# Performance work log

Hardware: AMD Instinct MI355X
Metric: run time of the kernel (lower is better)

Reference implementation:

```python
import jax, jax.numpy as jnp
import numpy as np

N = 50000      # nodes
E = 800000     # edges
F_IN = 128     # input node features
HID = 96       # hidden_channels (heads=1 -> in_dim=HID)
L = 4          # num_layers
OUT = 1
EPS_SM = 1e-16 # PyG softmax eps


def layer_norm(x, g, b):
    mu = jnp.mean(x, axis=-1, keepdims=True)
    var = jnp.var(x, axis=-1, keepdims=True)
    return (x - mu) * jax.lax.rsqrt(var + 1e-5) * g + b


def gatv2_layer(h, src, dst, ea, Wl, bl, Wr, br, We, att, bias):
    # GATv2Conv, heads=1, concat=True, add_self_loops=False, edge_dim=1
    xl = h @ Wl + bl                      # [N, C] source transform (x_j)
    xr = h @ Wr + br                      # [N, C] target transform (x_i)
    e = xl[src] + xr[dst] + ea @ We       # [E, C]
    e = jax.nn.leaky_relu(e, 0.2)
    alpha = e @ att                       # [E]
    # softmax over incoming edges of each destination node
    m = jax.ops.segment_max(alpha, dst, num_segments=N)
    a = jnp.exp(alpha - m[dst])
    s = jax.ops.segment_sum(a, dst, num_segments=N)
    a = a / (s[dst] + EPS_SM)
    out = jax.ops.segment_sum(xl[src] * a[:, None], dst, num_segments=N)
    return out + bias


def setup_inputs() -> dict:
    key = jax.random.key(0)
    ks = jax.random.split(key, 24)
    sc_in = 1.0 / np.sqrt(F_IN)
    sc_h = 1.0 / np.sqrt(HID)
    inp = {
        "x": jax.random.normal(ks[0], (N, F_IN), jnp.float32),
        "edge_index": jax.random.randint(ks[1], (2, E), 0, N, jnp.int64),
        "edge_weight": jax.random.uniform(ks[2], (E,), jnp.float32),
        "enc_W": jax.random.normal(ks[3], (F_IN, HID), jnp.float32) * sc_in,
        "enc_b": jnp.zeros((HID,), jnp.float32),
        "Wl": jax.random.normal(ks[4], (L, HID, HID), jnp.float32) * sc_h,
        "bl": jnp.zeros((L, HID), jnp.float32),
        "Wr": jax.random.normal(ks[5], (L, HID, HID), jnp.float32) * sc_h,
        "br": jnp.zeros((L, HID), jnp.float32),
        "We": jax.random.normal(ks[6], (L, 1, HID), jnp.float32),
        "att": jax.random.normal(ks[7], (L, HID), jnp.float32) * sc_h,
        "bias": jnp.zeros((L, HID), jnp.float32),
        "ln_g": jnp.ones((L, HID), jnp.float32),
        "ln_b": jnp.zeros((L, HID), jnp.float32),
        "lnf_g": jnp.ones((HID,), jnp.float32),
        "lnf_b": jnp.zeros((HID,), jnp.float32),
        "fc_W": jax.random.normal(ks[8], (HID, OUT), jnp.float32) * sc_h,
        "fc_b": jnp.zeros((OUT,), jnp.float32),
    }
    return inp


def reference(x, edge_index, edge_weight, enc_W, enc_b, Wl, bl, Wr, br, We, att,
              bias, ln_g, ln_b, lnf_g, lnf_b, fc_W, fc_b):
    src, dst = edge_index[0], edge_index[1]
    ea = edge_weight[:, None]             # [E, 1] edge_attr
    h = x @ enc_W + enc_b                 # node encoder
    for i in range(L):                    # DeepGCNLayer block='res+'
        hn = jax.nn.relu(layer_norm(h, ln_g[i], ln_b[i]))
        h = h + gatv2_layer(hn, src, dst, ea, Wl[i], bl[i], Wr[i], br[i],
                            We[i], att[i], bias[i])
    h = jax.nn.relu(layer_norm(h, lnf_g, lnf_b))
    return h @ fc_W + fc_b
```

## Files before the change

kernel.cpp:

```cpp
#include <hip/hip_runtime.h>
#include <math.h>

#define NN 50000
#define EE 800000
#define FIN 128
#define HID 96
#define NL 4
#define CHUNK 1024

typedef __attribute__((ext_vector_type(8))) short short8;
typedef __attribute__((ext_vector_type(4))) float floatx4;
typedef __attribute__((ext_vector_type(2))) _Float16 half2v;

#define WPREP_L (NL * 2 * 9216)
#define WPREP_TOT (WPREP_L + 12288)

__device__ __forceinline__ unsigned short f32_to_bf16_rne(float x) {
    unsigned u = __float_as_uint(x);
    unsigned r = (u + 0x7FFFu + ((u >> 16) & 1u)) >> 16;
    return (unsigned short)r;
}
__device__ __forceinline__ float bf16_to_f32(unsigned short h) {
    return __uint_as_float(((unsigned)h) << 16);
}

__global__ void k_hist(const int* __restrict__ dst, int* __restrict__ deg, int E) {
    int e = blockIdx.x * blockDim.x + threadIdx.x;
    if (e < E) atomicAdd(&deg[dst[e]], 1);
}

__global__ void k_scan1(const int* __restrict__ deg, int* __restrict__ partials, int n) {
    __shared__ int lds[256];
    int t = threadIdx.x;
    int base = blockIdx.x * CHUNK + t * 4;
    int s = 0;
    #pragma unroll
    for (int q = 0; q < 4; q++) { int idx = base + q; if (idx < n) s += deg[idx]; }
    lds[t] = s; __syncthreads();
    for (int o = 128; o > 0; o >>= 1) { if (t < o) lds[t] += lds[t + o]; __syncthreads(); }
    if (t == 0) partials[blockIdx.x] = lds[0];
}

__global__ void k_scan_mid(int* partials, int nb, int* rowptr, int n) {
    int lane = threadIdx.x;
    int orig = (lane < nb) ? partials[lane] : 0;
    int v = orig;
    #pragma unroll
    for (int off = 1; off < 64; off <<= 1) {
        int u = __shfl_up(v, off);
        if (lane >= off) v += u;
    }
    if (lane < nb) partials[lane] = v - orig;
    if (lane == 63) rowptr[n] = v;
}

__global__ void k_scan3(const int* __restrict__ deg, const int* __restrict__ partials,
                        int* __restrict__ rowptr, int* __restrict__ cursor, int n) {
    __shared__ int lds[256];
    int t = threadIdx.x;
    int base = blockIdx.x * CHUNK + t * 4;
    int v[4];
    #pragma unroll
    for (int q = 0; q < 4; q++) { int idx = base + q; v[q] = (idx < n) ? deg[idx] : 0; }
    int tsum = v[0] + v[1] + v[2] + v[3];
    lds[t] = tsum; __syncthreads();
    for (int o = 1; o < 256; o <<= 1) {
        int add = (t >= o) ? lds[t - o] : 0;
        __syncthreads();
        lds[t] += add;
        __syncthreads();
    }
    int excl = lds[t] - tsum;
    int run = partials[blockIdx.x] + excl;
    #pragma unroll
    for (int q = 0; q < 4; q++) {
        int idx = base + q;
        if (idx < n) { rowptr[idx] = run; cursor[idx] = run; run += v[q]; }
    }
}

__global__ void k_scatter(const int* __restrict__ src, const int* __restrict__ dst,
                          const float* __restrict__ ew, int* __restrict__ cursor,
                          uint2* __restrict__ epack, int E) {
    int e = blockIdx.x * blockDim.x + threadIdx.x;
    if (e < E) {
        int p = atomicAdd(&cursor[dst[e]], 1);
        epack[p] = make_uint2((unsigned)src[e], __float_as_uint(ew[e]));
    }
}

__global__ void k_wprep_all(const float* __restrict__ Wl, const float* __restrict__ Wr,
                            const float* __restrict__ encW,
                            unsigned short* __restrict__ wf_hi, unsigned short* __restrict__ wf_lo,
                            unsigned short* __restrict__ we_hi, unsigned short* __restrict__ we_lo) {
    int t = blockIdx.x * blockDim.x + threadIdx.x;
    if (t < WPREP_L) {
        int within = t % 9216, pair = t / 9216;
        int lr = pair & 1, layer = pair >> 1;
        int j = within & 7;
        int lane = (within >> 3) & 63;
        int cs = within >> 9;
        int s = cs % 3, ct = cs / 3;
        int col = ct * 16 + (lane & 15);
        int k = s * 32 + (lane >> 4) * 8 + j;
        const float* W = (lr ? Wr : Wl) + (size_t)layer * HID * HID;
        float v = W[k * HID + col];
        unsigned short hi = f32_to_bf16_rne(v);
        wf_hi[t] = hi;
        wf_lo[t] = f32_to_bf16_rne(v - bf16_to_f32(hi));
    } else if (t < WPREP_TOT) {
        int u = t - WPREP_L;
        int j = u & 7;
        int lane = (u >> 3) & 63;
        int cs = u >> 9;
        int s = cs & 3, ct = cs >> 2;
        int col = ct * 16 + (lane & 15);
        int k = s * 32 + (lane >> 4) * 8 + j;
        float v = encW[k * HID + col];
        unsigned short hi = f32_to_bf16_rne(v);
        we_hi[u] = hi;
        we_lo[u] = f32_to_bf16_rne(v - bf16_to_f32(hi));
    }
}

__global__ __launch_bounds__(256) void k_enc_mfma(const float* __restrict__ x,
        const unsigned short* __restrict__ we_hi, const unsigned short* __restrict__ we_lo,
        const float* __restrict__ b,
        const float* __restrict__ lng, const float* __restrict__ lnb,
        float* __restrict__ h,
        unsigned short* __restrict__ hn_hi, unsigned short* __restrict__ hn_lo, int n) {
    int t = threadIdx.x;
    int wave = t >> 6, lane = t & 63;
    int quad = lane >> 4, lid = lane & 15;
    int r0 = blockIdx.x * 64 + wave * 16;
    int arow = r0 + lid; if (arow >= n) arow = n - 1;
    short8 aH[4], aL[4];
    #pragma unroll
    for (int s = 0; s < 4; s++) {
        float4 p0 = *(const float4*)(x + (size_t)arow * FIN + s * 32 + quad * 8);
        float4 p1 = *(const float4*)(x + (size_t)arow * FIN + s * 32 + quad * 8 + 4);
        float f[8] = {p0.x, p0.y, p0.z, p0.w, p1.x, p1.y, p1.z, p1.w};
        #pragma unroll
        for (int j = 0; j < 8; j++) {
            unsigned short hi = f32_to_bf16_rne(f[j]);
            aH[s][j] = (short)hi;
            aL[s][j] = (short)f32_to_bf16_rne(f[j] - bf16_to_f32(hi));
        }
    }
    floatx4 o[6];
    #pragma unroll
    for (int ct = 0; ct < 6; ct++) {
        floatx4 acc = {0.f, 0.f, 0.f, 0.f};
        #pragma unroll
        for (int s = 0; s < 4; s++) {
            short8 bH = *(const short8*)(we_hi + ((ct * 4 + s) * 64 + lane) * 8);
            short8 bL = *(const short8*)(we_lo + ((ct * 4 + s) * 64 + lane) * 8);
            acc = __builtin_amdgcn_mfma_f32_16x16x32_bf16(aH[s], bH, acc, 0, 0, 0);
            acc = __builtin_amdgcn_mfma_f32_16x16x32_bf16(aH[s], bL, acc, 0, 0, 0);
            acc = __builtin_amdgcn_mfma_f32_16x16x32_bf16(aL[s], bH, acc, 0, 0, 0);
        }
        float bv = b[ct * 16 + lid];
        #pragma unroll
        for (int rg = 0; rg < 4; rg++) o[ct][rg] = acc[rg] + bv;
    }
    #pragma unroll
    for (int rg = 0; rg < 4; rg++) {
        float s1 = 0.f, s2 = 0.f;
        #pragma unroll
        for (int ct = 0; ct < 6; ct++) { s1 += o[ct][rg]; s2 += o[ct][rg] * o[ct][rg]; }
        #pragma unroll
        for (int off = 1; off < 16; off <<= 1) {
            s1 += __shfl_xor(s1, off);
            s2 += __shfl_xor(s2, off);
        }
        float mu = s1 * (1.f / 96.f);
        float var = s2 * (1.f / 96.f) - mu * mu;
        float rs = rsqrtf(var + 1e-5f);
        int orow = r0 + quad * 4 + rg;
        if (orow < n) {
            #pragma unroll
            for (int ct = 0; ct < 6; ct++) {
                int col = ct * 16 + lid;
                float v = o[ct][rg];
                h[(size_t)orow * HID + col] = v;
                float y = fmaxf((v - mu) * rs * lng[col] + lnb[col], 0.f);
                unsigned short hi = f32_to_bf16_rne(y);
                hn_hi[(size_t)orow * HID + col] = hi;
                hn_lo[(size_t)orow * HID + col] = f32_to_bf16_rne(y - bf16_to_f32(hi));
            }
        }
    }
}

__global__ __launch_bounds__(256) void k_gemm2_mfma(
        const unsigned short* __restrict__ hn_hi, const unsigned short* __restrict__ hn_lo,
        const unsigned short* __restrict__ wf_hi, const unsigned short* __restrict__ wf_lo,
        const float* __restrict__ bl, const float* __restrict__ br,
        unsigned short* __restrict__ xl_h, unsigned short* __restrict__ xr_h, int n) {
    int t = threadIdx.x;
    int wave = t >> 6, lane = t & 63;
    int quad = lane >> 4, lid = lane & 15;
    int r0 = blockIdx.x * 64 + wave * 16;
    int arow = r0 + lid; if (arow >= n) arow = n - 1;
    short8 aH[3], aL[3];
    #pragma unroll
    for (int s = 0; s < 3; s++) {
        aH[s] = *(const short8*)(hn_hi + (size_t)arow * HID + s * 32 + quad * 8);
        aL[s] = *(const short8*)(hn_lo + (size_t)arow * HID + s * 32 + quad * 8);
    }
    #pragma unroll
    for (int lr = 0; lr < 2; lr++) {
        const unsigned short* sh = wf_hi + lr * 9216;
        const unsigned short* sl = wf_lo + lr * 9216;
        const float* bias = lr ? br : bl;
        unsigned short* out = lr ? xr_h : xl_h;
        #pragma unroll
        for (int ct = 0; ct < 6; ct++) {
            floatx4 acc = {0.f, 0.f, 0.f, 0.f};
            #pragma unroll
            for (int s = 0; s < 3; s++) {
                short8 bH = *(const short8*)(sh + ((ct * 3 + s) * 64 + lane) * 8);
                short8 bL = *(const short8*)(sl + ((ct * 3 + s) * 64 + lane) * 8);
                acc = __builtin_amdgcn_mfma_f32_16x16x32_bf16(aH[s], bH, acc, 0, 0, 0);
                acc = __builtin_amdgcn_mfma_f32_16x16x32_bf16(aH[s], bL, acc, 0, 0, 0);
                acc = __builtin_amdgcn_mfma_f32_16x16x32_bf16(aL[s], bH, acc, 0, 0, 0);
            }
            int col = ct * 16 + lid;
            float bv = bias[col];
            #pragma unroll
            for (int rg = 0; rg < 4; rg++) {
                int orow = r0 + quad * 4 + rg;
                if (orow < n) {
                    _Float16 hv = (_Float16)(acc[rg] + bv);
                    out[(size_t)orow * HID + col] = *(unsigned short*)&hv;
                }
            }
        }
    }
}

__global__ __launch_bounds__(256) void k_gat_fused(
        const unsigned short* __restrict__ xl_h, const unsigned short* __restrict__ xr_h,
        const uint2* __restrict__ ep, const int* __restrict__ rowptr,
        const float* __restrict__ We, const float* __restrict__ att, const float* __restrict__ bias,
        float* __restrict__ h,
        unsigned short* __restrict__ hn_hi, unsigned short* __restrict__ hn_lo,
        float* __restrict__ out_final,
        const float* __restrict__ g, const float* __restrict__ bt,
        const float* __restrict__ fcW, const float* __restrict__ fcb,
        int mode, int n) {
    int lane = threadIdx.x & 63;
    int node = blockIdx.x * 4 + (threadIdx.x >> 6);
    if (node >= n) return;
    int grp = lane >> 4, sub = lane & 15;
    bool act = sub < 12;
    int d0 = sub * 8;
    unsigned gOffB = (unsigned)((act ? sub : 11) * 16);

    const float LOG2E = 1.4426950408889634f;
    half2v we_h[4], at_h[4], xr_hv[4];
    {
        union U8i { uint4 u; half2v h2[4]; };
        U8i xrw;
        xrw.u = *(const uint4*)((const char*)xr_h + ((unsigned)node * 192u + gOffB));
        if (act) {
            float4 a0 = *(const float4*)(We + d0),  a1 = *(const float4*)(We + d0 + 4);
            float4 c0 = *(const float4*)(att + d0), c1 = *(const float4*)(att + d0 + 4);
            we_h[0] = half2v{(_Float16)a0.x, (_Float16)a0.y}; we_h[1] = half2v{(_Float16)a0.z, (_Float16)a0.w};
            we_h[2] = half2v{(_Float16)a1.x, (_Float16)a1.y}; we_h[3] = half2v{(_Float16)a1.z, (_Float16)a1.w};
            at_h[0] = half2v{(_Float16)(c0.x*LOG2E), (_Float16)(c0.y*LOG2E)};
            at_h[1] = half2v{(_Float16)(c0.z*LOG2E), (_Float16)(c0.w*LOG2E)};
            at_h[2] = half2v{(_Float16)(c1.x*LOG2E), (_Float16)(c1.y*LOG2E)};
            at_h[3] = half2v{(_Float16)(c1.z*LOG2E), (_Float16)(c1.w*LOG2E)};
            #pragma unroll
            for (int j = 0; j < 4; j++) xr_hv[j] = xrw.h2[j];
        } else {
            #pragma unroll
            for (int j = 0; j < 4; j++) {
                we_h[j] = half2v{(_Float16)0.f, (_Float16)0.f};
                at_h[j] = we_h[j]; xr_hv[j] = we_h[j];
            }
        }
    }
    const half2v c02 = half2v{(_Float16)0.2f, (_Float16)0.2f};

    int beg = rowptr[node], end = rowptr[node + 1];
    float ssum = 0.f;
    float acc[8];
    #pragma unroll
    for (int j = 0; j < 8; j++) acc[j] = 0.f;

    union U8 { uint4 u; half2v h2[4]; _Float16 hf[8]; };

    auto lq = [&](int p, uint4& vraw, float& w, bool& val) {
        int pe = p + grp;
        val = pe < end;
        int pc = val ? pe : end - 1;
        uint2 e = ep[pc];
        w = __uint_as_float(e.y);
        vraw = *(const uint4*)((const char*)xl_h + (e.x * 192u + gOffB));
    };
    auto proc = [&](const uint4& vraw, float w, bool val) {
        U8 cv; cv.u = vraw;
        _Float16 wh = (_Float16)w;
        half2v w2 = half2v{wh, wh};
        float q = 0.f;
        #pragma unroll
        for (int j = 0; j < 4; j++) {
            half2v t = cv.h2[j] + xr_hv[j];
            t = w2 * we_h[j] + t;
            half2v t2 = t * c02;
            t = __builtin_elementwise_max(t, t2);
#if __has_builtin(__builtin_amdgcn_fdot2)
            q = __builtin_amdgcn_fdot2(t, at_h[j], q, false);
#else
            q = fmaf((float)t[0], (float)at_h[j][0], q);
            q = fmaf((float)t[1], (float)at_h[j][1], q);
#endif
        }
        q += __shfl_xor(q, 1); q += __shfl_xor(q, 2);
        q += __shfl_xor(q, 4); q += __shfl_xor(q, 8);
        float e = val ? exp2f(q) : 0.f;
        ssum += e;
        #pragma unroll
        for (int j = 0; j < 8; j++) acc[j] = fmaf((float)cv.hf[j], e, acc[j]);
    };

    if (beg < end) {
        uint4 vA, vB; float wA, wB; bool okA, okB;
        lq(beg,     vA, wA, okA);
        lq(beg + 4, vB, wB, okB);
        for (int p = beg; p < end; p += 8) {
            proc(vA, wA, okA);
            lq(p + 8, vA, wA, okA);
            proc(vB, wB, okB);
            lq(p + 12, vB, wB, okB);
        }
    }

    ssum += __shfl_xor(ssum, 16); ssum += __shfl_xor(ssum, 32);
    #pragma unroll
    for (int j = 0; j < 8; j++) {
        acc[j] += __shfl_xor(acc[j], 16);
        acc[j] += __shfl_xor(acc[j], 32);
    }
    float inv = 1.f / (ssum + 1e-16f);

    float nh[8];
    float s1 = 0.f, s2 = 0.f;
    if (act) {
        float4 h0 = *(const float4*)(h + (size_t)node * HID + d0);
        float4 h1 = *(const float4*)(h + (size_t)node * HID + d0 + 4);
        float4 b0 = *(const float4*)(bias + d0);
        float4 b1 = *(const float4*)(bias + d0 + 4);
        float hv[8] = {h0.x,h0.y,h0.z,h0.w,h1.x,h1.y,h1.z,h1.w};
        float bv[8] = {b0.x,b0.y,b0.z,b0.w,b1.x,b1.y,b1.z,b1.w};
        #pragma unroll
        for (int j = 0; j < 8; j++) {
            nh[j] = hv[j] + acc[j] * inv + bv[j];
            s1 += nh[j];
            s2 += nh[j] * nh[j];
        }
    } else {
        #pragma unroll
        for (int j = 0; j < 8; j++) nh[j] = 0.f;
    }
    #pragma unroll
    for (int off = 1; off < 16; off <<= 1) {
        s1 += __shfl_xor(s1, off);
        s2 += __shfl_xor(s2, off);
    }
    float mu = s1 * (1.f / 96.f);
    float var = s2 * (1.f / 96.f) - mu * mu;
    float rs = rsqrtf(var + 1e-5f);

    if (mode == 0) {
        if (grp == 0 && act) {
            float4 g0 = *(const float4*)(g + d0),  g1 = *(const float4*)(g + d0 + 4);
            float4 t0 = *(const float4*)(bt + d0), t1 = *(const float4*)(bt + d0 + 4);
            float gv[8] = {g0.x,g0.y,g0.z,g0.w,g1.x,g1.y,g1.z,g1.w};
            float tv[8] = {t0.x,t0.y,t0.z,t0.w,t1.x,t1.y,t1.z,t1.w};
            *(float4*)(h + (size_t)node * HID + d0)     = make_float4(nh[0], nh[1], nh[2], nh[3]);
            *(float4*)(h + (size_t)node * HID + d0 + 4) = make_float4(nh[4], nh[5], nh[6], nh[7]);
            unsigned hi[4], lo[4];
            #pragma unroll
            for (int j = 0; j < 4; j++) {
                float ox = fmaxf((nh[2*j]   - mu) * rs * gv[2*j]   + tv[2*j],   0.f);
                float oy = fmaxf((nh[2*j+1] - mu) * rs * gv[2*j+1] + tv[2*j+1], 0.f);
                unsigned short hx = f32_to_bf16_rne(ox), hy = f32_to_bf16_rne(oy);
                unsigned short lx = f32_to_bf16_rne(ox - bf16_to_f32(hx));
                unsigned short ly = f32_to_bf16_rne(oy - bf16_to_f32(hy));
                hi[j] = (unsigned)hx | ((unsigned)hy << 16);
                lo[j] = (unsigned)lx | ((unsigned)ly << 16);
            }
            *(uint4*)(hn_hi + (size_t)node * HID + d0) = make_uint4(hi[0], hi[1], hi[2], hi[3]);
            *(uint4*)(hn_lo + (size_t)node * HID + d0) = make_uint4(lo[0], lo[1], lo[2], lo[3]);
        }
    } else {
        float pacc = 0.f;
        if (act) {
            float4 g0 = *(const float4*)(g + d0),  g1 = *(const float4*)(g + d0 + 4);
            float4 t0 = *(const float4*)(bt + d0), t1 = *(const float4*)(bt + d0 + 4);
            float4 w0 = *(const float4*)(fcW + d0), w1 = *(const float4*)(fcW + d0 + 4);
            float gv[8] = {g0.x,g0.y,g0.z,g0.w,g1.x,g1.y,g1.z,g1.w};
            float tv[8] = {t0.x,t0.y,t0.z,t0.w,t1.x,t1.y,t1.z,t1.w};
            float wv[8] = {w0.x,w0.y,w0.z,w0.w,w1.x,w1.y,w1.z,w1.w};
            #pragma unroll
            for (int j = 0; j < 8; j++) {
                float y = fmaxf((nh[j] - mu) * rs * gv[j] + tv[j], 0.f);
                pacc = fmaf(y, wv[j], pacc);
            }
        }
        #pragma unroll
        for (int off = 1; off < 16; off <<= 1) pacc += __shfl_xor(pacc, off);
        if (lane == 0) out_final[node] = pacc + fcb[0];
    }
}

extern "C" void kernel_launch(void* const* d_in, const int* in_sizes, int n_in,
                              void* d_out, int out_size, void* d_ws, size_t ws_size,
                              hipStream_t stream) {
    const float* x    = (const float*)d_in[0];
    const int*   ei   = (const int*)  d_in[1];
    const float* ew   = (const float*)d_in[2];
    const float* encW = (const float*)d_in[3];
    const float* encB = (const float*)d_in[4];
    const float* Wl   = (const float*)d_in[5];
    const float* bl   = (const float*)d_in[6];
    const float* Wr   = (const float*)d_in[7];
    const float* br   = (const float*)d_in[8];
    const float* We   = (const float*)d_in[9];
    const float* att  = (const float*)d_in[10];
    const float* bias = (const float*)d_in[11];
    const float* lng  = (const float*)d_in[12];
    const float* lnb  = (const float*)d_in[13];
    const float* lnfg = (const float*)d_in[14];
    const float* lnfb = (const float*)d_in[15];
    const float* fcW  = (const float*)d_in[16];
    const float* fcb  = (const float*)d_in[17];
    float* out = (float*)d_out;

    const int* src = ei;
    const int* dst = ei + EE;

    char* ws = (char*)d_ws;
    size_t off = 0;
    auto alloc = [&](size_t bytes) -> void* {
        void* p = ws + off;
        off += (bytes + 255) & ~(size_t)255;
        return p;
    };
    float* h      = (float*)alloc((size_t)NN * HID * 4);
    unsigned short* xl_h  = (unsigned short*)alloc((size_t)NN * HID * 2 + 256);
    unsigned short* xr_h  = (unsigned short*)alloc((size_t)NN * HID * 2 + 256);
    unsigned short* hn_hi = (unsigned short*)alloc((size_t)NN * HID * 2);
    unsigned short* hn_lo = (unsigned short*)alloc((size_t)NN * HID * 2);
    unsigned short* wf_hi = (unsigned short*)alloc((size_t)WPREP_L * 2);
    unsigned short* wf_lo = (unsigned short*)alloc((size_t)WPREP_L * 2);
    unsigned short* we_hi = (unsigned short*)alloc(12288 * 2);
    unsigned short* we_lo = (unsigned short*)alloc(12288 * 2);
    int*   deg    = (int*)  alloc((size_t)NN * 4);
    int*   rowptr = (int*)  alloc((size_t)(NN + 1) * 4);
    int*   cursor = (int*)  alloc((size_t)NN * 4);
    uint2* epack  = (uint2*)alloc((size_t)EE * 8);
    int*   parts  = (int*)  alloc(256 * 4);

    const int NB = (NN + CHUNK - 1) / CHUNK;
    const int EB = (EE + 255) / 256;
    const int MB = (NN + 63) / 64;
    const int WB = (NN + 3) / 4;

    hipMemsetAsync(deg, 0, (size_t)NN * 4, stream);
    k_hist<<<EB, 256, 0, stream>>>(dst, deg, EE);
    k_scan1<<<NB, 256, 0, stream>>>(deg, parts, NN);
    k_scan_mid<<<1, 64, 0, stream>>>(parts, NB, rowptr, NN);
    k_scan3<<<NB, 256, 0, stream>>>(deg, parts, rowptr, cursor, NN);
    k_scatter<<<EB, 256, 0, stream>>>(src, dst, ew, cursor, epack, EE);

    k_wprep_all<<<(WPREP_TOT + 255) / 256, 256, 0, stream>>>(Wl, Wr, encW, wf_hi, wf_lo, we_hi, we_lo);

    k_enc_mfma<<<MB, 256, 0, stream>>>(x, we_hi, we_lo, encB, lng, lnb, h, hn_hi, hn_lo, NN);

    for (int l = 0; l < NL; l++) {
        k_gemm2_mfma<<<MB, 256, 0, stream>>>(hn_hi, hn_lo,
            wf_hi + (size_t)l * 2 * 9216, wf_lo + (size_t)l * 2 * 9216,
            bl + l * HID, br + l * HID, xl_h, xr_h, NN);
        if (l < NL - 1) {
            k_gat_fused<<<WB, 256, 0, stream>>>(xl_h, xr_h, epack, rowptr,
                We + l * HID, att + l * HID, bias + l * HID,
                h, hn_hi, hn_lo, (float*)nullptr,
                lng + (l + 1) * HID, lnb + (l + 1) * HID,
                (const float*)nullptr, (const float*)nullptr, 0, NN);
        } else {
            k_gat_fused<<<WB, 256, 0, stream>>>(xl_h, xr_h, epack, rowptr,
                We + l * HID, att + l * HID, bias + l * HID,
                h, (unsigned short*)nullptr, (unsigned short*)nullptr, out,
                lnfg, lnfb, fcW, fcb, 1, NN);
        }
    }
}
```

Measured before the change: 509.5 us.

## Use all 16 lanes with 6 features each in GAT gather; stage GEMM weights in LDS

The fused GAT kernel now maps the 96 features onto all 16 lanes of each group, 6 halves (12 bytes) per lane, instead of 12 active lanes with 8 halves each. This removes idle lanes and the act branches, at the cost of 12-byte loads and stores that may be less efficient than 16-byte vectors. Separately, the bf16 MFMA GEMM kernel copies the Wl/Wr hi/lo weight fragments into shared memory once per block, then reads B operands from LDS instead of global memory. The staging adds two barriers per weight matrix and 36KB of LDS per block, which may lower occupancy.

New measurement: 476.5 us. 6.5% less time.

```diff
diff --git a/kernel.cpp b/kernel.cpp
--- a/kernel.cpp
+++ b/kernel.cpp
@@ -14,6 +14,8 @@
 
 #define WPREP_L (NL * 2 * 9216)
 #define WPREP_TOT (WPREP_L + 12288)
+
+struct u96 { unsigned x, y, z; };
 
 __device__ __forceinline__ unsigned short f32_to_bf16_rne(float x) {
     unsigned u = __float_as_uint(x);
@@ -197,6 +199,8 @@
         const unsigned short* __restrict__ wf_hi, const unsigned short* __restrict__ wf_lo,
         const float* __restrict__ bl, const float* __restrict__ br,
         unsigned short* __restrict__ xl_h, unsigned short* __restrict__ xr_h, int n) {
+    __shared__ unsigned short lh[9216];
+    __shared__ unsigned short ll[9216];
     int t = threadIdx.x;
     int wave = t >> 6, lane = t & 63;
     int quad = lane >> 4, lid = lane & 15;
@@ -208,10 +212,15 @@
         aH[s] = *(const short8*)(hn_hi + (size_t)arow * HID + s * 32 + quad * 8);
         aL[s] = *(const short8*)(hn_lo + (size_t)arow * HID + s * 32 + quad * 8);
     }
-    #pragma unroll
     for (int lr = 0; lr < 2; lr++) {
         const unsigned short* sh = wf_hi + lr * 9216;
         const unsigned short* sl = wf_lo + lr * 9216;
+        __syncthreads();
+        for (int u = t; u < 1152; u += 256) {
+            *(short8*)(lh + u * 8) = *(const short8*)(sh + u * 8);
+            *(short8*)(ll + u * 8) = *(const short8*)(sl + u * 8);
+        }
+        __syncthreads();
         const float* bias = lr ? br : bl;
         unsigned short* out = lr ? xr_h : xl_h;
         #pragma unroll
@@ -219,8 +228,8 @@
             floatx4 acc = {0.f, 0.f, 0.f, 0.f};
             #pragma unroll
             for (int s = 0; s < 3; s++) {
-                short8 bH = *(const short8*)(sh + ((ct * 3 + s) * 64 + lane) * 8);
-                short8 bL = *(const short8*)(sl + ((ct * 3 + s) * 64 + lane) * 8);
+                short8 bH = *(const short8*)(lh + ((ct * 3 + s) * 64 + lane) * 8);
+                short8 bL = *(const short8*)(ll + ((ct * 3 + s) * 64 + lane) * 8);
                 acc = __builtin_amdgcn_mfma_f32_16x16x32_bf16(aH[s], bH, acc, 0, 0, 0);
                 acc = __builtin_amdgcn_mfma_f32_16x16x32_bf16(aH[s], bL, acc, 0, 0, 0);
                 acc = __builtin_amdgcn_mfma_f32_16x16x32_bf16(aL[s], bH, acc, 0, 0, 0);
@@ -253,60 +262,53 @@
     int node = blockIdx.x * 4 + (threadIdx.x >> 6);
     if (node >= n) return;
     int grp = lane >> 4, sub = lane & 15;
-    bool act = sub < 12;
-    int d0 = sub * 8;
-    unsigned gOffB = (unsigned)((act ? sub : 11) * 16);
+    int d0 = sub * 6;
+    unsigned gOffB = (unsigned)(sub * 12);
 
     const float LOG2E = 1.4426950408889634f;
-    half2v we_h[4], at_h[4], xr_hv[4];
+    union U6 { u96 u; half2v h2[3]; _Float16 hf[6]; };
+    half2v we_h[3], at_h[3], xr_hv[3];
     {
-        union U8i { uint4 u; half2v h2[4]; };
-        U8i xrw;
-        xrw.u = *(const uint4*)((const char*)xr_h + ((unsigned)node * 192u + gOffB));
-        if (act) {
-            float4 a0 = *(const float4*)(We + d0),  a1 = *(const float4*)(We + d0 + 4);
-            float4 c0 = *(const float4*)(att + d0), c1 = *(const float4*)(att + d0 + 4);
-            we_h[0] = half2v{(_Float16)a0.x, (_Float16)a0.y}; we_h[1] = half2v{(_Float16)a0.z, (_Float16)a0.w};
-            we_h[2] = half2v{(_Float16)a1.x, (_Float16)a1.y}; we_h[3] = half2v{(_Float16)a1.z, (_Float16)a1.w};
-            at_h[0] = half2v{(_Float16)(c0.x*LOG2E), (_Float16)(c0.y*LOG2E)};
-            at_h[1] = half2v{(_Float16)(c0.z*LOG2E), (_Float16)(c0.w*LOG2E)};
-            at_h[2] = half2v{(_Float16)(c1.x*LOG2E), (_Float16)(c1.y*LOG2E)};
-            at_h[3] = half2v{(_Float16)(c1.z*LOG2E), (_Float16)(c1.w*LOG2E)};
-            #pragma unroll
-            for (int j = 0; j < 4; j++) xr_hv[j] = xrw.h2[j];
-        } else {
-            #pragma unroll
-            for (int j = 0; j < 4; j++) {
-                we_h[j] = half2v{(_Float16)0.f, (_Float16)0.f};
-                at_h[j] = we_h[j]; xr_hv[j] = we_h[j];
-            }
-        }
+        U6 xrw;
+        xrw.u = *(const u96*)((const char*)xr_h + ((unsigned)node * 192u + gOffB));
+        float2 a0 = *(const float2*)(We + d0);
+        float2 a1 = *(const float2*)(We + d0 + 2);
+        float2 a2 = *(const float2*)(We + d0 + 4);
+        float2 c0 = *(const float2*)(att + d0);
+        float2 c1 = *(const float2*)(att + d0 + 2);
+        float2 c2 = *(const float2*)(att + d0 + 4);
+        we_h[0] = half2v{(_Float16)a0.x, (_Float16)a0.y};
+        we_h[1] = half2v{(_Float16)a1.x, (_Float16)a1.y};
+        we_h[2] = half2v{(_Float16)a2.x, (_Float16)a2.y};
+        at_h[0] = half2v{(_Float16)(c0.x*LOG2E), (_Float16)(c0.y*LOG2E)};
+        at_h[1] = half2v{(_Float16)(c1.x*LOG2E), (_Float16)(c1.y*LOG2E)};
+        at_h[2] = half2v{(_Float16)(c2.x*LOG2E), (_Float16)(c2.y*LOG2E)};
+        #pragma unroll
+        for (int j = 0; j < 3; j++) xr_hv[j] = xrw.h2[j];
     }
     const half2v c02 = half2v{(_Float16)0.2f, (_Float16)0.2f};
 
     int beg = rowptr[node], end = rowptr[node + 1];
     float ssum = 0.f;
-    float acc[8];
-    #pragma unroll
-    for (int j = 0; j < 8; j++) acc[j] = 0.f;
-
-    union U8 { uint4 u; half2v h2[4]; _Float16 hf[8]; };
-
-    auto lq = [&](int p, uint4& vraw, float& w, bool& val) {
+    float acc[6];
+    #pragma unroll
+    for (int j = 0; j < 6; j++) acc[j] = 0.f;
+
+    auto lq = [&](int p, u96& vraw, float& w, bool& val) {
         int pe = p + grp;
         val = pe < end;
         int pc = val ? pe : end - 1;
         uint2 e = ep[pc];
         w = __uint_as_float(e.y);
-        vraw = *(const uint4*)((const char*)xl_h + (e.x * 192u + gOffB));
+        vraw = *(const u96*)((const char*)xl_h + (e.x * 192u + gOffB));
     };
-    auto proc = [&](const uint4& vraw, float w, bool val) {
-        U8 cv; cv.u = vraw;
+    auto proc = [&](const u96& vraw, float w, bool val) {
+        U6 cv; cv.u = vraw;
         _Float16 wh = (_Float16)w;
         half2v w2 = half2v{wh, wh};
         float q = 0.f;
         #pragma unroll
-        for (int j = 0; j < 4; j++) {
+        for (int j = 0; j < 3; j++) {
             half2v t = cv.h2[j] + xr_hv[j];
             t = w2 * we_h[j] + t;
             half2v t2 = t * c02;
@@ -323,11 +325,11 @@
         float e = val ? exp2f(q) : 0.f;
         ssum += e;
         #pragma unroll
-        for (int j = 0; j < 8; j++) acc[j] = fmaf((float)cv.hf[j], e, acc[j]);
+        for (int j = 0; j < 6; j++) acc[j] = fmaf((float)cv.hf[j], e, acc[j]);
     };
 
     if (beg < end) {
-        uint4 vA, vB; float wA, wB; bool okA, okB;
+        u96 vA, vB; float wA, wB; bool okA, okB;
         lq(beg,     vA, wA, okA);
         lq(beg + 4, vB, wB, okB);
         for (int p = beg; p < end; p += 8) {
@@ -340,30 +342,29 @@
 
     ssum += __shfl_xor(ssum, 16); ssum += __shfl_xor(ssum, 32);
     #pragma unroll
-    for (int j = 0; j < 8; j++) {
+    for (int j = 0; j < 6; j++) {
         acc[j] += __shfl_xor(acc[j], 16);
         acc[j] += __shfl_xor(acc[j], 32);
     }
     float inv = 1.f / (ssum + 1e-16f);
 
-    float nh[8];
+    float nh[6];
     float s1 = 0.f, s2 = 0.f;
-    if (act) {
-        float4 h0 = *(const float4*)(h + (size_t)node * HID + d0);
-        float4 h1 = *(const float4*)(h + (size_t)node * HID + d0 + 4);
-        float4 b0 = *(const float4*)(bias + d0);
-        float4 b1 = *(const float4*)(bias + d0 + 4);
-        float hv[8] = {h0.x,h0.y,h0.z,h0.w,h1.x,h1.y,h1.z,h1.w};
-        float bv[8] = {b0.x,b0.y,b0.z,b0.w,b1.x,b1.y,b1.z,b1.w};
-        #pragma unroll
-        for (int j = 0; j < 8; j++) {
+    {
+        float2 h0 = *(const float2*)(h + (size_t)node * HID + d0);
+        float2 h1 = *(const float2*)(h + (size_t)node * HID + d0 + 2);
+        float2 h2 = *(const float2*)(h + (size_t)node * HID + d0 + 4);
+        float2 b0 = *(const float2*)(bias + d0);
+        float2 b1 = *(const float2*)(bias + d0 + 2);
+        float2 b2 = *(const float2*)(bias + d0 + 4);
+        float hv[6] = {h0.x, h0.y, h1.x, h1.y, h2.x, h2.y};
+        float bv[6] = {b0.x, b0.y, b1.x, b1.y, b2.x, b2.y};
+        #pragma unroll
+        for (int j = 0; j < 6; j++) {
             nh[j] = hv[j] + acc[j] * inv + bv[j];
             s1 += nh[j];
             s2 += nh[j] * nh[j];
         }
-    } else {
-        #pragma unroll
-        for (int j = 0; j < 8; j++) nh[j] = 0.f;
     }
     #pragma unroll
     for (int off = 1; off < 16; off <<= 1) {
@@ -375,16 +376,21 @@
     float rs = rsqrtf(var + 1e-5f);
 
     if (mode == 0) {
-        if (grp == 0 && act) {
-            float4 g0 = *(const float4*)(g + d0),  g1 = *(const float4*)(g + d0 + 4);
-            float4 t0 = *(const float4*)(bt + d0), t1 = *(const float4*)(bt + d0 + 4);
-            float gv[8] = {g0.x,g0.y,g0.z,g0.w,g1.x,g1.y,g1.z,g1.w};
-            float tv[8] = {t0.x,t0.y,t0.z,t0.w,t1.x,t1.y,t1.z,t1.w};
-            *(float4*)(h + (size_t)node * HID + d0)     = make_float4(nh[0], nh[1], nh[2], nh[3]);
-            *(float4*)(h + (size_t)node * HID + d0 + 4) = make_float4(nh[4], nh[5], nh[6], nh[7]);
-            unsigned hi[4], lo[4];
+        if (grp == 0) {
+            float2 g0 = *(const float2*)(g + d0);
+            float2 g1 = *(const float2*)(g + d0 + 2);
+            float2 g2 = *(const float2*)(g + d0 + 4);
+            float2 t0 = *(const float2*)(bt + d0);
+            float2 t1 = *(const float2*)(bt + d0 + 2);
+            float2 t2 = *(const float2*)(bt + d0 + 4);
+            float gv[6] = {g0.x, g0.y, g1.x, g1.y, g2.x, g2.y};
+            float tv[6] = {t0.x, t0.y, t1.x, t1.y, t2.x, t2.y};
+            *(float2*)(h + (size_t)node * HID + d0)     = make_float2(nh[0], nh[1]);
+            *(float2*)(h + (size_t)node * HID + d0 + 2) = make_float2(nh[2], nh[3]);
+            *(float2*)(h + (size_t)node * HID + d0 + 4) = make_float2(nh[4], nh[5]);
+            unsigned hi[3], lo[3];
             #pragma unroll
-            for (int j = 0; j < 4; j++) {
+            for (int j = 0; j < 3; j++) {
                 float ox = fmaxf((nh[2*j]   - mu) * rs * gv[2*j]   + tv[2*j],   0.f);
                 float oy = fmaxf((nh[2*j+1] - mu) * rs * gv[2*j+1] + tv[2*j+1], 0.f);
                 unsigned short hx = f32_to_bf16_rne(ox), hy = f32_to_bf16_rne(oy);
@@ -393,20 +399,28 @@
                 hi[j] = (unsigned)hx | ((unsigned)hy << 16);
                 lo[j] = (unsigned)lx | ((unsigned)ly << 16);
             }
-            *(uint4*)(hn_hi + (size_t)node * HID + d0) = make_uint4(hi[0], hi[1], hi[2], hi[3]);
-            *(uint4*)(hn_lo + (size_t)node * HID + d0) = make_uint4(lo[0], lo[1], lo[2], lo[3]);
+            u96 wh = {hi[0], hi[1], hi[2]};
+            u96 wl = {lo[0], lo[1], lo[2]};
+            *(u96*)((char*)hn_hi + 2 * ((size_t)node * HID + d0)) = wh;
+            *(u96*)((char*)hn_lo + 2 * ((size_t)node * HID + d0)) = wl;
         }
     } else {
         float pacc = 0.f;
-        if (act) {
-            float4 g0 = *(const float4*)(g + d0),  g1 = *(const float4*)(g + d0 + 4);
-            float4 t0 = *(const float4*)(bt + d0), t1 = *(const float4*)(bt + d0 + 4);
-            float4 w0 = *(const float4*)(fcW + d0), w1 = *(const float4*)(fcW + d0 + 4);
-            float gv[8] = {g0.x,g0.y,g0.z,g0.w,g1.x,g1.y,g1.z,g1.w};
-            float tv[8] = {t0.x,t0.y,t0.z,t0.w,t1.x,t1.y,t1.z,t1.w};
-            float wv[8] = {w0.x,w0.y,w0.z,w0.w,w1.x,w1.y,w1.z,w1.w};
+        {
+            float2 g0 = *(const float2*)(g + d0);
+            float2 g1 = *(const float2*)(g + d0 + 2);
+            float2 g2 = *(const float2*)(g + d0 + 4);
+            float2 t0 = *(const float2*)(bt + d0);
+            float2 t1 = *(const float2*)(bt + d0 + 2);
+            float2 t2 = *(const float2*)(bt + d0 + 4);
+            float2 w0 = *(const float2*)(fcW + d0);
+            float2 w1 = *(const float2*)(fcW + d0 + 2);
+            float2 w2 = *(const float2*)(fcW + d0 + 4);
+            float gv[6] = {g0.x, g0.y, g1.x, g1.y, g2.x, g2.y};
+            float tv[6] = {t0.x, t0.y, t1.x, t1.y, t2.x, t2.y};
+            float wv[6] = {w0.x, w0.y, w1.x, w1.y, w2.x, w2.y};
             #pragma unroll
-            for (int j = 0; j < 8; j++) {
+            for (int j = 0; j < 6; j++) {
                 float y = fmaxf((nh[j] - mu) * rs * gv[j] + tv[j], 0.f);
                 pacc = fmaf(y, wv[j], pacc);
             }
```
